# Optimization experiments

Hardware: AMD Instinct MI355X
Metric: run time of the kernel (lower is better)

The kernel has to match this reference:

```python
import jax, jax.numpy as jnp
import numpy as np

S, B, E, H = 2048, 4, 1024, 16
HD = E // H
EPS = 1e-8


def _bit_linear(x, W, b):
    """BitNetLinear (eval): ternary weight quant + abs-mean activation scaling."""
    w_scale = jnp.maximum(jnp.mean(jnp.abs(W)), EPS)
    wn = W / w_scale
    qw = jnp.sign(wn) * (jnp.abs(wn) > 0.5).astype(x.dtype)  # {-1,0,1}
    a_scale = jnp.maximum(jnp.mean(jnp.abs(x)), EPS)
    out = (x / a_scale) @ (qw * w_scale).T + b
    return out * a_scale


def setup_inputs() -> dict:
    key = jax.random.key(0)
    ks = jax.random.split(key, 9)
    # xavier-uniform-ish init for [E,E] weights
    lim = float(np.sqrt(6.0 / (E + E)))
    def w(k):
        return jax.random.uniform(k, (E, E), jnp.float32, -lim, lim)
    return {
        "query": jax.random.normal(ks[0], (S, B, E), jnp.float32),
        "Wq": w(ks[1]), "bq": jnp.zeros((E,), jnp.float32),
        "Wk": w(ks[2]), "bk": jnp.zeros((E,), jnp.float32),
        "Wv": w(ks[3]), "bv": jnp.zeros((E,), jnp.float32),
        "Wo": w(ks[4]), "bo": jnp.zeros((E,), jnp.float32),
    }


def reference(query, Wq, bq, Wk, bk, Wv, bv, Wo, bo):
    q = _bit_linear(query, Wq, bq)  # [S,B,E]
    k = _bit_linear(query, Wk, bk)
    v = _bit_linear(query, Wv, bv)
    # [S,B,E] -> [B*H, S, HD]
    def split_heads(t):
        return t.reshape(S, B * H, HD).transpose(1, 0, 2)
    q, k, v = split_heads(q), split_heads(k), split_heads(v)
    scaling = HD ** -0.5
    scores = jnp.einsum("nqd,nkd->nqk", q, k) * scaling  # [B*H,S,S]
    probs = jax.nn.softmax(scores, axis=-1)
    attn = jnp.einsum("nqk,nkd->nqd", probs, v)  # [B*H,S,HD]
    attn = attn.transpose(1, 0, 2).reshape(S, B, E)
    out = _bit_linear(attn, Wo, bo)  # [S,B,E]
    # need_weights=True, average_attn_weights=True -> mean over heads
    attn_weights = probs.reshape(B, H, S, S).mean(axis=1)  # [B,S,S]
    return out, attn_weights
```

## Files before the change

kernel.cpp:

```cpp
#include <hip/hip_runtime.h>


typedef __bf16 bf16_t;
typedef __bf16 bf16x8 __attribute__((ext_vector_type(8)));
typedef float  f32x4  __attribute__((ext_vector_type(4)));

#define MFMA16(Af, Bf, Cv) __builtin_amdgcn_mfma_f32_16x16x32_bf16((Af), (Bf), (Cv), 0, 0, 0)
#define EXP2(x) __builtin_amdgcn_exp2f(x)

constexpr float LOG2E   = 1.4426950408889634f;
constexpr float SHIFT2  = 14.426950408889634f;
constexpr float QSCALE  = 0.125f * LOG2E;

__device__ __forceinline__ void gload16(const void* g, void* l) {
  __builtin_amdgcn_global_load_lds(
      (const __attribute__((address_space(1))) void*)g,
      (__attribute__((address_space(3))) void*)l, 16, 0, 0);
}

__device__ __forceinline__ void stage8k(const bf16_t* __restrict__ g0, int gstride,
                                        char* ldsb, int tid, int w) {
  const int rr = tid >> 3;
  const int cs = ((tid & 7) * 8) ^ ((rr & 7) * 8);
  gload16(g0 + (size_t)rr * gstride + cs, ldsb + w * 1024);
  gload16(g0 + (size_t)(rr + 32) * gstride + cs, ldsb + 4096 + w * 1024);
}

__device__ __forceinline__ bf16x8 lds_frag(const char* ldsb, int row, int bytecol) {
  return *(const bf16x8*)(ldsb + row * 128 + (bytecol ^ ((row & 7) << 4)));
}

constexpr int S_ = 2048, B_ = 4, E_ = 1024, H_ = 16, HD_ = 64;
constexpr int M_ = S_ * B_;
constexpr int NH_ = B_ * H_;

constexpr size_t OFF_SCALES = 0;
constexpr size_t OFF_PART   = 256;
constexpr size_t OFF_XB     = 8192;
constexpr size_t SZ_X       = (size_t)M_ * E_ * 2;
constexpr size_t OFF_TQKV   = OFF_XB + SZ_X;
constexpr size_t OFF_TO     = OFF_TQKV + (size_t)3072 * 1024 * 2;
constexpr size_t OFF_QH     = OFF_TO + (size_t)1024 * 1024 * 2;
constexpr size_t SZ_HD      = (size_t)NH_ * S_ * HD_ * 2;
constexpr size_t OFF_KH     = OFF_QH + SZ_HD;
constexpr size_t OFF_VT     = OFF_KH + SZ_HD;
constexpr size_t OFF_STL    = OFF_VT + SZ_HD;
constexpr size_t OFF_ATTN   = OFF_STL + (size_t)NH_ * S_ * 4;

__global__ void k_abs_sum_f32(const float4* __restrict__ src, int n4, float* __restrict__ out) {
  float s = 0.f;
  for (int i = blockIdx.x * blockDim.x + threadIdx.x; i < n4; i += gridDim.x * blockDim.x) {
    float4 x = src[i];
    s += fabsf(x.x) + fabsf(x.y) + fabsf(x.z) + fabsf(x.w);
  }
  __shared__ float red[256];
  red[threadIdx.x] = s; __syncthreads();
  for (int st = 128; st > 0; st >>= 1) {
    if (threadIdx.x < st) red[threadIdx.x] += red[threadIdx.x + st];
    __syncthreads();
  }
  if (threadIdx.x == 0) out[blockIdx.x] = red[0];
}

__global__ void k_abs_sum_bf16(const bf16x8* __restrict__ src, int n8, float* __restrict__ out) {
  float s = 0.f;
  for (int i = blockIdx.x * blockDim.x + threadIdx.x; i < n8; i += gridDim.x * blockDim.x) {
    bf16x8 x = src[i];
    #pragma unroll
    for (int e = 0; e < 8; ++e) s += fabsf((float)x[e]);
  }
  __shared__ float red[256];
  red[threadIdx.x] = s; __syncthreads();
  for (int st = 128; st > 0; st >>= 1) {
    if (threadIdx.x < st) red[threadIdx.x] += red[threadIdx.x + st];
    __syncthreads();
  }
  if (threadIdx.x == 0) out[blockIdx.x] = red[0];
}

__global__ void k_finalize(const float* __restrict__ part, float* __restrict__ scales,
                           int r0, int r1) {
  __shared__ float red[256];
  int t = threadIdx.x;
  for (int r = r0; r < r1; ++r) {
    red[t] = part[r * 256 + t];
    __syncthreads();
    for (int st = 128; st > 0; st >>= 1) {
      if (t < st) red[t] += red[t + st];
      __syncthreads();
    }
    if (t == 0) {
      float cnt = (r < 4) ? 1048576.0f : 8388608.0f;
      scales[r] = fmaxf(red[0] / cnt, 1e-8f);
    }
    __syncthreads();
  }
}

__device__ __forceinline__ unsigned short tern_u(float w, float wsc) {
  float wn = w / wsc;
  if (!(fabsf(wn) > 0.5f)) return 0;
  return (wn > 0.f) ? (unsigned short)0x3F80 : (unsigned short)0xBF80;
}

__global__ void k_quantize(const float4* __restrict__ W, const float* __restrict__ scales,
                           int seg, ushort4* __restrict__ T) {
  int i = blockIdx.x * 256 + threadIdx.x;
  float wsc = scales[seg];
  float4 w = W[i];
  ushort4 o;
  o.x = tern_u(w.x, wsc); o.y = tern_u(w.y, wsc);
  o.z = tern_u(w.z, wsc); o.w = tern_u(w.w, wsc);
  T[i] = o;
}

__global__ void k_cvt_x(const float4* __restrict__ X, ushort4* __restrict__ Xb) {
  int i = blockIdx.x * 256 + threadIdx.x;
  float4 v = X[i];
  ushort4 h;
  h.x = __builtin_bit_cast(unsigned short, (__bf16)v.x);
  h.y = __builtin_bit_cast(unsigned short, (__bf16)v.y);
  h.z = __builtin_bit_cast(unsigned short, (__bf16)v.z);
  h.w = __builtin_bit_cast(unsigned short, (__bf16)v.w);
  Xb[i] = h;
}

__global__ __launch_bounds__(256) void k_gemm_qkv(
    const bf16_t* __restrict__ Xb, const bf16_t* __restrict__ T,
    const float* __restrict__ scales,
    const float* __restrict__ bq, const float* __restrict__ bk, const float* __restrict__ bv,
    bf16_t* __restrict__ Qh, bf16_t* __restrict__ Kh, bf16_t* __restrict__ Vt) {
  __shared__ char lds[32768];
  const int tid = threadIdx.x, w = tid >> 6, lane = tid & 63;
  const int g = lane >> 4, cc = lane & 15;
  const int l = blockIdx.x;
  const int xcd = l & 7, r = l >> 3;
  const int nIdx = r % 24, mloc = r / 24;
  const int bm = (xcd * 8 + mloc) * 128, bn = nIdx * 128;
  const int wm = (w >> 1) * 64, wn = (w & 1) * 64;
  const int subA = wm >> 6, subB = wn >> 6;
  f32x4 acc[4][4] = {};
  for (int kt = 0; kt < 16; ++kt) {
    const int k0 = kt * 64;
    const bf16_t* xa = &Xb[(size_t)bm * 1024 + k0];
    const bf16_t* tb = &T[(size_t)bn * 1024 + k0];
    stage8k(xa, 1024, lds, tid, w);
    stage8k(xa + 64 * 1024, 1024, lds + 8192, tid, w);
    stage8k(tb, 1024, lds + 16384, tid, w);
    stage8k(tb + 64 * 1024, 1024, lds + 24576, tid, w);
    __syncthreads();
    const char* As = lds + subA * 8192;
    const char* Bs = lds + 16384 + subB * 8192;
    #pragma unroll
    for (int ks = 0; ks < 2; ++ks) {
      bf16x8 af[4], bfr[4];
      #pragma unroll
      for (int i = 0; i < 4; ++i)
        af[i] = lds_frag(As, (wm & 63) + i * 16 + cc, ks * 64 + g * 16);
      #pragma unroll
      for (int j = 0; j < 4; ++j)
        bfr[j] = lds_frag(Bs, (wn & 63) + j * 16 + cc, ks * 64 + g * 16);
      __builtin_amdgcn_s_setprio(1);
      #pragma unroll
      for (int i = 0; i < 4; ++i)
        #pragma unroll
        for (int j = 0; j < 4; ++j)
          acc[i][j] = MFMA16(af[i], bfr[j], acc[i][j]);
      __builtin_amdgcn_s_setprio(0);
    }
    __syncthreads();
  }
  const int seg = bn >> 10;
  const float wsc = scales[seg];
  const float asx = scales[4];
  const float* bias = (seg == 0) ? bq : (seg == 1) ? bk : bv;
  #pragma unroll
  for (int i = 0; i < 4; ++i)
    #pragma unroll
    for (int j = 0; j < 4; ++j)
      #pragma unroll
      for (int r2 = 0; r2 < 4; ++r2) {
        int m = bm + wm + i * 16 + g * 4 + r2;
        int n = bn + wn + j * 16 + cc;
        int e = n & 1023;
        float v = acc[i][j][r2] * wsc + bias[e] * asx;
        int s = m >> 2, b = m & 3, h = e >> 6, d = e & 63;
        if (seg == 0) {
          Qh[((b * 16 + h) * 2048 + s) * 64 + d] = (bf16_t)(v * QSCALE);
        } else if (seg == 1) {
          Kh[((b * 16 + h) * 2048 + s) * 64 + d] = (bf16_t)v;
        } else {
          Vt[((b * 16 + h) * 64 + d) * 2048 + s] = (bf16_t)v;
        }
      }
}

__global__ __launch_bounds__(256) void k_flash(
    const bf16_t* __restrict__ Qh, const bf16_t* __restrict__ Kh,
    const bf16_t* __restrict__ Vt,
    bf16_t* __restrict__ attnb, float* __restrict__ stl) {
  __shared__ char lds[2 * 16384 + 16384];
  char* Ps = lds + 32768;
  const int tid = threadIdx.x, w = tid >> 6, lane = tid & 63;
  const int g = lane >> 4, cc = lane & 15;
  const int l = blockIdx.x;
  const int head = (l & 7) * 8 + ((l >> 3) & 7);
  const int q0 = (l >> 6) * 128;
  const int qbaseA = (head * 2048 + q0 + w * 32 + cc) * 64 + g * 8;
  const int qbaseB = qbaseA + 16 * 64;
  const bf16x8 qa0 = *(const bf16x8*)&Qh[qbaseA];
  const bf16x8 qa1 = *(const bf16x8*)&Qh[qbaseA + 32];
  const bf16x8 qb0 = *(const bf16x8*)&Qh[qbaseB];
  const bf16x8 qb1 = *(const bf16x8*)&Qh[qbaseB + 32];
  const bf16_t* Kb = Kh + (size_t)head * 2048 * 64;
  const bf16_t* Vb = Vt + (size_t)head * 64 * 2048;
  const bf16_t one_b = (bf16_t)1.0f;
  const bf16x8 ones = {one_b, one_b, one_b, one_b, one_b, one_b, one_b, one_b};
  const f32x4 minit = {-SHIFT2, -SHIFT2, -SHIFT2, -SHIFT2};
  f32x4 accOA[4] = {}, accOB[4] = {};
  f32x4 accLA = {}, accLB = {};
  stage8k(Kb, 64, lds, tid, w);
  stage8k(Vb, 2048, lds + 8192, tid, w);
  __syncthreads();
  int cur = 0;
  for (int kt0 = 0; kt0 < 2048; kt0 += 64) {
    if (kt0 + 64 < 2048) {
      char* nb = lds + (cur ^ 1) * 16384;
      stage8k(Kb + (kt0 + 64) * 64, 64, nb, tid, w);
      stage8k(Vb + (kt0 + 64), 2048, nb + 8192, tid, w);
    }
    const char* KhL = lds + cur * 16384;
    const char* VtL = KhL + 8192;
    f32x4 sA[4], sB[4];
    #pragma unroll
    for (int nf = 0; nf < 4; ++nf) { sA[nf] = minit; sB[nf] = minit; }
    __builtin_amdgcn_s_setprio(1);
    #pragma unroll
    for (int nf = 0; nf < 4; ++nf) {
      const int row = nf * 16 + cc;
      bf16x8 kh0 = lds_frag(KhL, row, g * 16);
      bf16x8 kh1 = lds_frag(KhL, row, 64 + g * 16);
      sA[nf] = MFMA16(qa0, kh0, sA[nf]);
      sA[nf] = MFMA16(qa1, kh1, sA[nf]);
      sB[nf] = MFMA16(qb0, kh0, sB[nf]);
      sB[nf] = MFMA16(qb1, kh1, sB[nf]);
    }
    __builtin_amdgcn_s_setprio(0);
    #pragma unroll
    for (int nf = 0; nf < 4; ++nf)
      #pragma unroll
      for (int r = 0; r < 4; ++r) {
        float pA = EXP2(sA[nf][r]);
        float pB = EXP2(sB[nf][r]);
        int rowA = w * 32 + g * 4 + r;
        int rowB = rowA + 16;
        int colb = (nf * 16 + cc) * 2;
        *(bf16_t*)(Ps + ((rowA * 128 + colb) ^ ((rowA & 7) << 4))) = (bf16_t)pA;
        *(bf16_t*)(Ps + ((rowB * 128 + colb) ^ ((rowB & 7) << 4))) = (bf16_t)pB;
      }
    const int prA = w * 32 + cc, prB = prA + 16;
    const int pbA = (prA * 128 + g * 16) ^ ((prA & 7) << 4);
    const int pbB = (prB * 128 + g * 16) ^ ((prB & 7) << 4);
    const bf16x8 paA0 = *(const bf16x8*)(Ps + pbA);
    const bf16x8 paA1 = *(const bf16x8*)(Ps + (pbA ^ 64));
    const bf16x8 paB0 = *(const bf16x8*)(Ps + pbB);
    const bf16x8 paB1 = *(const bf16x8*)(Ps + (pbB ^ 64));
    __builtin_amdgcn_s_setprio(1);
    accLA = MFMA16(paA0, ones, accLA);
    accLA = MFMA16(paA1, ones, accLA);
    accLB = MFMA16(paB0, ones, accLB);
    accLB = MFMA16(paB1, ones, accLB);
    #pragma unroll
    for (int df = 0; df < 4; ++df) {
      const int row = df * 16 + cc;
      bf16x8 v0 = lds_frag(VtL, row, g * 16);
      bf16x8 v1 = lds_frag(VtL, row, 64 + g * 16);
      accOA[df] = MFMA16(paA0, v0, accOA[df]);
      accOA[df] = MFMA16(paA1, v1, accOA[df]);
      accOB[df] = MFMA16(paB0, v0, accOB[df]);
      accOB[df] = MFMA16(paB1, v1, accOB[df]);
    }
    __builtin_amdgcn_s_setprio(0);
    __syncthreads();
    cur ^= 1;
  }
  const int b = head >> 4, h = head & 15;
  #pragma unroll
  for (int df = 0; df < 4; ++df)
    #pragma unroll
    for (int r = 0; r < 4; ++r) {
      int qA = q0 + w * 32 + g * 4 + r;
      int e = h * 64 + df * 16 + cc;
      attnb[(qA * 4 + b) * 1024 + e] = (bf16_t)(accOA[df][r] / accLA[r]);
      attnb[((qA + 16) * 4 + b) * 1024 + e] = (bf16_t)(accOB[df][r] / accLB[r]);
    }
  if (cc == 0) {
    #pragma unroll
    for (int r = 0; r < 4; ++r) {
      int qA = q0 + w * 32 + g * 4 + r;
      stl[head * 2048 + qA] = accLA[r];
      stl[head * 2048 + qA + 16] = accLB[r];
    }
  }
}

__global__ __launch_bounds__(256) void k_pm(
    const bf16_t* __restrict__ Qh, const bf16_t* __restrict__ Kh,
    const float* __restrict__ stl, float* __restrict__ aw) {
  __shared__ char kbuf[2 * 16384];
  __shared__ float sc_[2048];
  const int tid = threadIdx.x, w = tid >> 6, lane = tid & 63;
  const int g = lane >> 4, cc = lane & 15;
  const int l = blockIdx.x;
  const int q0 = (l & 15) * 128, b = (l >> 4) & 3, z = l >> 6;
  const int kbeg = z * 128;
  for (int i = tid; i < 2048; i += 256) {
    int h = i >> 7, q = i & 127;
    sc_[i] = -log2f(stl[(b * 16 + h) * 2048 + q0 + q]) - SHIFT2;
  }
  stage8k(Kh + ((size_t)(b * 16 + 0) * 2048 + kbeg) * 64, 64, kbuf, tid, w);
  stage8k(Kh + ((size_t)(b * 16 + 1) * 2048 + kbeg) * 64, 64, kbuf + 8192, tid, w);
  __syncthreads();
  int cur = 0;
  float pmA[4][4], pmB[4][4];
  for (int it = 0; it < 16; ++it) {
    const int kt = it >> 3, hp = it & 7;
    const int ktl = kbeg + kt * 64;
    if (it < 15) {
      const int nx = it + 1;
      const int ktn = kbeg + (nx >> 3) * 64, hpn = nx & 7;
      char* nb = kbuf + (cur ^ 1) * 16384;
      stage8k(Kh + ((size_t)(b * 16 + 2 * hpn) * 2048 + ktn) * 64, 64, nb, tid, w);
      stage8k(Kh + ((size_t)(b * 16 + 2 * hpn + 1) * 2048 + ktn) * 64, 64, nb + 8192, tid, w);
    }
    if (hp == 0) {
      #pragma unroll
      for (int nf = 0; nf < 4; ++nf)
        #pragma unroll
        for (int r = 0; r < 4; ++r) { pmA[nf][r] = 0.f; pmB[nf][r] = 0.f; }
    }
    #pragma unroll
    for (int hi = 0; hi < 2; ++hi) {
      const int h = 2 * hp + hi;
      const int head = b * 16 + h;
      const int qbaseA = (head * 2048 + q0 + w * 32 + cc) * 64 + g * 8;
      const int qbaseB = qbaseA + 16 * 64;
      bf16x8 qa0 = *(const bf16x8*)&Qh[qbaseA];
      bf16x8 qa1 = *(const bf16x8*)&Qh[qbaseA + 32];
      bf16x8 qb0 = *(const bf16x8*)&Qh[qbaseB];
      bf16x8 qb1 = *(const bf16x8*)&Qh[qbaseB + 32];
      f32x4 ciA, ciB;
      #pragma unroll
      for (int r = 0; r < 4; ++r) {
        int qloc = w * 32 + g * 4 + r;
        ciA[r] = sc_[h * 128 + qloc];
        ciB[r] = sc_[h * 128 + qloc + 16];
      }
      const char* KhL = kbuf + cur * 16384 + hi * 8192;
      f32x4 sA[4], sB[4];
      #pragma unroll
      for (int nf = 0; nf < 4; ++nf) { sA[nf] = ciA; sB[nf] = ciB; }
      __builtin_amdgcn_s_setprio(1);
      #pragma unroll
      for (int nf = 0; nf < 4; ++nf) {
        const int row = nf * 16 + cc;
        bf16x8 kh0 = lds_frag(KhL, row, g * 16);
        bf16x8 kh1 = lds_frag(KhL, row, 64 + g * 16);
        sA[nf] = MFMA16(qa0, kh0, sA[nf]);
        sA[nf] = MFMA16(qa1, kh1, sA[nf]);
        sB[nf] = MFMA16(qb0, kh0, sB[nf]);
        sB[nf] = MFMA16(qb1, kh1, sB[nf]);
      }
      __builtin_amdgcn_s_setprio(0);
      #pragma unroll
      for (int nf = 0; nf < 4; ++nf)
        #pragma unroll
        for (int r = 0; r < 4; ++r) {
          pmA[nf][r] += EXP2(sA[nf][r]);
          pmB[nf][r] += EXP2(sB[nf][r]);
        }
    }
    if (hp == 7) {
      #pragma unroll
      for (int nf = 0; nf < 4; ++nf)
        #pragma unroll
        for (int r = 0; r < 4; ++r) {
          int qA = q0 + w * 32 + g * 4 + r;
          int k = ktl + nf * 16 + cc;
          aw[((long)(b * 2048 + qA)) * 2048 + k] = pmA[nf][r] * 0.0625f;
          aw[((long)(b * 2048 + qA + 16)) * 2048 + k] = pmB[nf][r] * 0.0625f;
        }
    }
    __syncthreads();
    cur ^= 1;
  }
}

__global__ __launch_bounds__(256) void k_gemm_out(
    const bf16_t* __restrict__ A, const bf16_t* __restrict__ T,
    const float* __restrict__ scales, const float* __restrict__ bo,
    float* __restrict__ out) {
  __shared__ char lds[32768];
  const int tid = threadIdx.x, w = tid >> 6, lane = tid & 63;
  const int g = lane >> 4, cc = lane & 15;
  const int l = blockIdx.x;
  const int xcd = l & 7, r = l >> 3;
  const int nIdx = r & 7, mloc = r >> 3;
  const int bm = (xcd * 8 + mloc) * 128, bn = nIdx * 128;
  const int wm = (w >> 1) * 64, wn = (w & 1) * 64;
  const int subA = wm >> 6, subB = wn >> 6;
  f32x4 acc[4][4] = {};
  for (int kt = 0; kt < 16; ++kt) {
    const int k0 = kt * 64;
    const bf16_t* aa = &A[(size_t)bm * 1024 + k0];
    const bf16_t* tb = &T[(size_t)bn * 1024 + k0];
    stage8k(aa, 1024, lds, tid, w);
    stage8k(aa + 64 * 1024, 1024, lds + 8192, tid, w);
    stage8k(tb, 1024, lds + 16384, tid, w);
    stage8k(tb + 64 * 1024, 1024, lds + 24576, tid, w);
    __syncthreads();
    const char* As = lds + subA * 8192;
    const char* Bs = lds + 16384 + subB * 8192;
    #pragma unroll
    for (int ks = 0; ks < 2; ++ks) {
      bf16x8 af[4], bfr[4];
      #pragma unroll
      for (int i = 0; i < 4; ++i)
        af[i] = lds_frag(As, (wm & 63) + i * 16 + cc, ks * 64 + g * 16);
      #pragma unroll
      for (int j = 0; j < 4; ++j)
        bfr[j] = lds_frag(Bs, (wn & 63) + j * 16 + cc, ks * 64 + g * 16);
      __builtin_amdgcn_s_setprio(1);
      #pragma unroll
      for (int i = 0; i < 4; ++i)
        #pragma unroll
        for (int j = 0; j < 4; ++j)
          acc[i][j] = MFMA16(af[i], bfr[j], acc[i][j]);
      __builtin_amdgcn_s_setprio(0);
    }
    __syncthreads();
  }
  const float wsc = scales[3], asa = scales[5];
  #pragma unroll
  for (int i = 0; i < 4; ++i)
    #pragma unroll
    for (int j = 0; j < 4; ++j)
      #pragma unroll
      for (int r2 = 0; r2 < 4; ++r2) {
        int m = bm + wm + i * 16 + g * 4 + r2;
        int n = bn + wn + j * 16 + cc;
        out[m * 1024 + n] = acc[i][j][r2] * wsc + bo[n] * asa;
      }
}

extern "C" void kernel_launch(void* const* d_in, const int* in_sizes, int n_in,
                              void* d_out, int out_size, void* d_ws, size_t ws_size,
                              hipStream_t stream) {
  (void)in_sizes; (void)n_in; (void)out_size; (void)ws_size;
  const float* query = (const float*)d_in[0];
  const float* Wq = (const float*)d_in[1];
  const float* bq = (const float*)d_in[2];
  const float* Wk = (const float*)d_in[3];
  const float* bk = (const float*)d_in[4];
  const float* Wv = (const float*)d_in[5];
  const float* bv = (const float*)d_in[6];
  const float* Wo = (const float*)d_in[7];
  const float* bo = (const float*)d_in[8];

  char* ws = (char*)d_ws;
  float*  scales = (float*)(ws + OFF_SCALES);
  float*  part   = (float*)(ws + OFF_PART);
  bf16_t* Xb     = (bf16_t*)(ws + OFF_XB);
  bf16_t* Tqkv   = (bf16_t*)(ws + OFF_TQKV);
  bf16_t* To     = (bf16_t*)(ws + OFF_TO);
  bf16_t* Qh     = (bf16_t*)(ws + OFF_QH);
  bf16_t* Kh     = (bf16_t*)(ws + OFF_KH);
  bf16_t* Vt     = (bf16_t*)(ws + OFF_VT);
  float*  Stl    = (float*)(ws + OFF_STL);
  bf16_t* Attn   = (bf16_t*)(ws + OFF_ATTN);

  float* out0 = (float*)d_out;
  float* aw   = out0 + (size_t)M_ * E_;

  k_abs_sum_f32<<<256, 256, 0, stream>>>((const float4*)Wq, 262144, part);
  k_abs_sum_f32<<<256, 256, 0, stream>>>((const float4*)Wk, 262144, part + 256);
  k_abs_sum_f32<<<256, 256, 0, stream>>>((const float4*)Wv, 262144, part + 512);
  k_abs_sum_f32<<<256, 256, 0, stream>>>((const float4*)Wo, 262144, part + 768);
  k_abs_sum_f32<<<256, 256, 0, stream>>>((const float4*)query, 2097152, part + 1024);
  k_finalize<<<1, 256, 0, stream>>>(part, scales, 0, 5);

  k_quantize<<<1024, 256, 0, stream>>>((const float4*)Wq, scales, 0, (ushort4*)Tqkv);
  k_quantize<<<1024, 256, 0, stream>>>((const float4*)Wk, scales, 1, (ushort4*)(Tqkv + 1048576));
  k_quantize<<<1024, 256, 0, stream>>>((const float4*)Wv, scales, 2, (ushort4*)(Tqkv + 2097152));
  k_quantize<<<1024, 256, 0, stream>>>((const float4*)Wo, scales, 3, (ushort4*)To);
  k_cvt_x<<<8192, 256, 0, stream>>>((const float4*)query, (ushort4*)Xb);

  k_gemm_qkv<<<1536, 256, 0, stream>>>(Xb, Tqkv, scales, bq, bk, bv, Qh, Kh, Vt);
  k_flash<<<1024, 256, 0, stream>>>(Qh, Kh, Vt, Attn, Stl);
  k_pm<<<1024, 256, 0, stream>>>(Qh, Kh, Stl, aw);
  k_abs_sum_bf16<<<256, 256, 0, stream>>>((const bf16x8*)Attn, 1048576, part + 1280);
  k_finalize<<<1, 256, 0, stream>>>(part, scales, 5, 6);
  k_gemm_out<<<512, 256, 0, stream>>>(Attn, To, scales, bo, out0);
}
```

Baseline: 339.2 us.

## Fuse prep kernels and widen flash attention blocks to 512 threads

Merges the four weight abs-sum launches into one kernel and the four quantize launches into one, and fuses the query bf16 conversion with its abs-sum reduction so the input is read once. The flash-attention kernel now runs 512-thread blocks covering 256 query rows. All eight waves share each staged K/V tile, which halves K/V staging traffic per query and reduces block count. The larger LDS footprint (64KB) and larger blocks may reduce occupancy, and the flash index math (q0 with w up to 7) must stay consistent with the hidden epilogue.

New measurement: 309.5 us. -8.8%, faster.

```diff
diff --git a/kernel.cpp b/kernel.cpp
--- a/kernel.cpp
+++ b/kernel.cpp
@@ -24,6 +24,13 @@
   const int cs = ((tid & 7) * 8) ^ ((rr & 7) * 8);
   gload16(g0 + (size_t)rr * gstride + cs, ldsb + w * 1024);
   gload16(g0 + (size_t)(rr + 32) * gstride + cs, ldsb + 4096 + w * 1024);
+}
+
+__device__ __forceinline__ void stage8k512(const bf16_t* __restrict__ g0, int gstride,
+                                           char* ldsb, int tid) {
+  const int rr = tid >> 3;
+  const int cs = ((tid & 7) * 8) ^ ((rr & 7) * 8);
+  gload16(g0 + (size_t)rr * gstride + cs, ldsb + (tid >> 6) * 1024);
 }
 
 __device__ __forceinline__ bf16x8 lds_frag(const char* ldsb, int row, int bytecol) {
@@ -47,9 +54,13 @@
 constexpr size_t OFF_STL    = OFF_VT + SZ_HD;
 constexpr size_t OFF_ATTN   = OFF_STL + (size_t)NH_ * S_ * 4;
 
-__global__ void k_abs_sum_f32(const float4* __restrict__ src, int n4, float* __restrict__ out) {
+__global__ void k_abs_sum_w4(const float4* __restrict__ W0, const float4* __restrict__ W1,
+                             const float4* __restrict__ W2, const float4* __restrict__ W3,
+                             float* __restrict__ part) {
+  const int seg = blockIdx.x >> 8, blk = blockIdx.x & 255;
+  const float4* src = (seg == 0) ? W0 : (seg == 1) ? W1 : (seg == 2) ? W2 : W3;
   float s = 0.f;
-  for (int i = blockIdx.x * blockDim.x + threadIdx.x; i < n4; i += gridDim.x * blockDim.x) {
+  for (int i = blk * 256 + threadIdx.x; i < 262144; i += 65536) {
     float4 x = src[i];
     s += fabsf(x.x) + fabsf(x.y) + fabsf(x.z) + fabsf(x.w);
   }
@@ -59,7 +70,29 @@
     if (threadIdx.x < st) red[threadIdx.x] += red[threadIdx.x + st];
     __syncthreads();
   }
-  if (threadIdx.x == 0) out[blockIdx.x] = red[0];
+  if (threadIdx.x == 0) part[seg * 256 + blk] = red[0];
+}
+
+__global__ void k_prep_x(const float4* __restrict__ X, ushort4* __restrict__ Xb,
+                         float* __restrict__ part) {
+  float s = 0.f;
+  for (int i = blockIdx.x * 256 + threadIdx.x; i < 2097152; i += 65536) {
+    float4 v = X[i];
+    s += fabsf(v.x) + fabsf(v.y) + fabsf(v.z) + fabsf(v.w);
+    ushort4 h;
+    h.x = __builtin_bit_cast(unsigned short, (__bf16)v.x);
+    h.y = __builtin_bit_cast(unsigned short, (__bf16)v.y);
+    h.z = __builtin_bit_cast(unsigned short, (__bf16)v.z);
+    h.w = __builtin_bit_cast(unsigned short, (__bf16)v.w);
+    Xb[i] = h;
+  }
+  __shared__ float red[256];
+  red[threadIdx.x] = s; __syncthreads();
+  for (int st = 128; st > 0; st >>= 1) {
+    if (threadIdx.x < st) red[threadIdx.x] += red[threadIdx.x + st];
+    __syncthreads();
+  }
+  if (threadIdx.x == 0) part[blockIdx.x] = red[0];
 }
 
 __global__ void k_abs_sum_bf16(const bf16x8* __restrict__ src, int n8, float* __restrict__ out) {
@@ -103,26 +136,21 @@
   return (wn > 0.f) ? (unsigned short)0x3F80 : (unsigned short)0xBF80;
 }
 
-__global__ void k_quantize(const float4* __restrict__ W, const float* __restrict__ scales,
-                           int seg, ushort4* __restrict__ T) {
-  int i = blockIdx.x * 256 + threadIdx.x;
+__global__ void k_quantize4(const float4* __restrict__ W0, const float4* __restrict__ W1,
+                            const float4* __restrict__ W2, const float4* __restrict__ W3,
+                            const float* __restrict__ scales,
+                            ushort4* __restrict__ T0, ushort4* __restrict__ T1,
+                            ushort4* __restrict__ T2, ushort4* __restrict__ T3) {
+  const int seg = blockIdx.x >> 10;
+  const int i = (blockIdx.x & 1023) * 256 + threadIdx.x;
+  const float4* W = (seg == 0) ? W0 : (seg == 1) ? W1 : (seg == 2) ? W2 : W3;
+  ushort4* T = (seg == 0) ? T0 : (seg == 1) ? T1 : (seg == 2) ? T2 : T3;
   float wsc = scales[seg];
   float4 w = W[i];
   ushort4 o;
   o.x = tern_u(w.x, wsc); o.y = tern_u(w.y, wsc);
   o.z = tern_u(w.z, wsc); o.w = tern_u(w.w, wsc);
   T[i] = o;
-}
-
-__global__ void k_cvt_x(const float4* __restrict__ X, ushort4* __restrict__ Xb) {
-  int i = blockIdx.x * 256 + threadIdx.x;
-  float4 v = X[i];
-  ushort4 h;
-  h.x = __builtin_bit_cast(unsigned short, (__bf16)v.x);
-  h.y = __builtin_bit_cast(unsigned short, (__bf16)v.y);
-  h.z = __builtin_bit_cast(unsigned short, (__bf16)v.z);
-  h.w = __builtin_bit_cast(unsigned short, (__bf16)v.w);
-  Xb[i] = h;
 }
 
 __global__ __launch_bounds__(256) void k_gemm_qkv(
@@ -195,17 +223,17 @@
       }
 }
 
-__global__ __launch_bounds__(256) void k_flash(
+__global__ __launch_bounds__(512) void k_flash(
     const bf16_t* __restrict__ Qh, const bf16_t* __restrict__ Kh,
     const bf16_t* __restrict__ Vt,
     bf16_t* __restrict__ attnb, float* __restrict__ stl) {
-  __shared__ char lds[2 * 16384 + 16384];
+  __shared__ char lds[65536];
   char* Ps = lds + 32768;
   const int tid = threadIdx.x, w = tid >> 6, lane = tid & 63;
   const int g = lane >> 4, cc = lane & 15;
   const int l = blockIdx.x;
   const int head = (l & 7) * 8 + ((l >> 3) & 7);
-  const int q0 = (l >> 6) * 128;
+  const int q0 = (l >> 6) * 256;
   const int qbaseA = (head * 2048 + q0 + w * 32 + cc) * 64 + g * 8;
   const int qbaseB = qbaseA + 16 * 64;
   const bf16x8 qa0 = *(const bf16x8*)&Qh[qbaseA];
@@ -219,18 +247,17 @@
   const f32x4 minit = {-SHIFT2, -SHIFT2, -SHIFT2, -SHIFT2};
   f32x4 accOA[4] = {}, accOB[4] = {};
   f32x4 accLA = {}, accLB = {};
-  stage8k(Kb, 64, lds, tid, w);
-  stage8k(Vb, 2048, lds + 8192, tid, w);
+  stage8k512(Kb, 64, lds, tid);
+  stage8k512(Vb, 2048, lds + 16384, tid);
   __syncthreads();
   int cur = 0;
   for (int kt0 = 0; kt0 < 2048; kt0 += 64) {
     if (kt0 + 64 < 2048) {
-      char* nb = lds + (cur ^ 1) * 16384;
-      stage8k(Kb + (kt0 + 64) * 64, 64, nb, tid, w);
-      stage8k(Vb + (kt0 + 64), 2048, nb + 8192, tid, w);
-    }
-    const char* KhL = lds + cur * 16384;
-    const char* VtL = KhL + 8192;
+      stage8k512(Kb + (kt0 + 64) * 64, 64, lds + (cur ^ 1) * 8192, tid);
+      stage8k512(Vb + (kt0 + 64), 2048, lds + 16384 + (cur ^ 1) * 8192, tid);
+    }
+    const char* KhL = lds + cur * 8192;
+    const char* VtL = lds + 16384 + cur * 8192;
     f32x4 sA[4], sB[4];
     #pragma unroll
     for (int nf = 0; nf < 4; ++nf) { sA[nf] = minit; sB[nf] = minit; }
@@ -482,21 +509,17 @@
   float* out0 = (float*)d_out;
   float* aw   = out0 + (size_t)M_ * E_;
 
-  k_abs_sum_f32<<<256, 256, 0, stream>>>((const float4*)Wq, 262144, part);
-  k_abs_sum_f32<<<256, 256, 0, stream>>>((const float4*)Wk, 262144, part + 256);
-  k_abs_sum_f32<<<256, 256, 0, stream>>>((const float4*)Wv, 262144, part + 512);
-  k_abs_sum_f32<<<256, 256, 0, stream>>>((const float4*)Wo, 262144, part + 768);
-  k_abs_sum_f32<<<256, 256, 0, stream>>>((const float4*)query, 2097152, part + 1024);
+  k_abs_sum_w4<<<1024, 256, 0, stream>>>((const float4*)Wq, (const float4*)Wk,
+                                         (const float4*)Wv, (const float4*)Wo, part);
+  k_prep_x<<<256, 256, 0, stream>>>((const float4*)query, (ushort4*)Xb, part + 1024);
   k_finalize<<<1, 256, 0, stream>>>(part, scales, 0, 5);
-
-  k_quantize<<<1024, 256, 0, stream>>>((const float4*)Wq, scales, 0, (ushort4*)Tqkv);
-  k_quantize<<<1024, 256, 0, stream>>>((const float4*)Wk, scales, 1, (ushort4*)(Tqkv + 1048576));
-  k_quantize<<<1024, 256, 0, stream>>>((const float4*)Wv, scales, 2, (ushort4*)(Tqkv + 2097152));
-  k_quantize<<<1024, 256, 0, stream>>>((const float4*)Wo, scales, 3, (ushort4*)To);
-  k_cvt_x<<<8192, 256, 0, stream>>>((const float4*)query, (ushort4*)Xb);
+  k_quantize4<<<4096, 256, 0, stream>>>((const float4*)Wq, (const float4*)Wk,
+                                        (const float4*)Wv, (const float4*)Wo, scales,
+                                        (ushort4*)Tqkv, (ushort4*)(Tqkv + 1048576),
+                                        (ushort4*)(Tqkv + 2097152), (ushort4*)To);
 
   k_gemm_qkv<<<1536, 256, 0, stream>>>(Xb, Tqkv, scales, bq, bk, bv, Qh, Kh, Vt);
-  k_flash<<<1024, 256, 0, stream>>>(Qh, Kh, Vt, Attn, Stl);
+  k_flash<<<512, 512, 0, stream>>>(Qh, Kh, Vt, Attn, Stl);
   k_pm<<<1024, 256, 0, stream>>>(Qh, Kh, Stl, aw);
   k_abs_sum_bf16<<<256, 256, 0, stream>>>((const bf16x8*)Attn, 1048576, part + 1280);
   k_finalize<<<1, 256, 0, stream>>>(part, scales, 5, 6);
```
